# Kernel optimization log

Measured on AMD Instinct MI355X. Metric: run time of the kernel, lower is better.

Reference implementation:

```python
import jax, jax.numpy as jnp
import numpy as np

D = 1024
H = 16
DH = D // H
SCALE = 1.0 / float(np.sqrt(DH))
EPS = 1e-5


def layer_norm(x, g, b):
    mu = jnp.mean(x, axis=-1, keepdims=True)
    var = jnp.mean((x - mu) ** 2, axis=-1, keepdims=True)
    return (x - mu) * jax.lax.rsqrt(var + EPS) * g + b


def setup_inputs() -> dict:
    key = jax.random.key(0)
    ks = jax.random.split(key, 12)
    B, N = 2, 2048
    x = jax.random.normal(ks[0], (B, N, D), dtype=jnp.float32)
    # sparse 0/1 adjacency (tree-like density) plus self loops
    adj = (jax.random.uniform(ks[1], (B, N, N)) < 0.002).astype(jnp.float32)
    adj = jnp.maximum(adj, jnp.eye(N, dtype=jnp.float32)[None])
    attn_mask = jnp.zeros((B, N, N), dtype=jnp.float32)
    s = 0.02
    params = {
        "qkv_w": jax.random.normal(ks[2], (D, 3 * D)) * s,
        "qkv_b": jnp.zeros((3 * D,), jnp.float32),
        "out_w": jax.random.normal(ks[3], (D, D)) * s,
        "out_b": jnp.zeros((D,), jnp.float32),
        "ln1_g": jnp.ones((D,), jnp.float32),
        "ln1_b": jnp.zeros((D,), jnp.float32),
        "ln2_g": jnp.ones((D,), jnp.float32),
        "ln2_b": jnp.zeros((D,), jnp.float32),
        "ff1_w": jax.random.normal(ks[4], (D, 4 * D)) * s,
        "ff1_b": jnp.zeros((4 * D,), jnp.float32),
        "ff2_w": jax.random.normal(ks[5], (4 * D, D)) * s,
        "ff2_b": jnp.zeros((D,), jnp.float32),
        "struct_bias": jnp.zeros((1,), jnp.float32) + 0.1,
    }
    return {"x": x, "adjacency": adj, "attn_mask": attn_mask, **params}


def reference(x, adjacency, attn_mask, qkv_w, qkv_b, out_w, out_b,
              ln1_g, ln1_b, ln2_g, ln2_b, ff1_w, ff1_b, ff2_w, ff2_b,
              struct_bias):
    b, n, d = x.shape
    residual = x
    h = layer_norm(x, ln1_g, ln1_b)
    qkv = (h @ qkv_w + qkv_b).reshape(b, n, 3, H, DH)
    q = jnp.transpose(qkv[:, :, 0], (0, 2, 1, 3))  # [B,H,N,Dh]
    k = jnp.transpose(qkv[:, :, 1], (0, 2, 1, 3))
    v = jnp.transpose(qkv[:, :, 2], (0, 2, 1, 3))
    scores = jnp.einsum("bhqd,bhkd->bhqk", q, k) * SCALE
    scores = scores + struct_bias[0] * adjacency[:, None] + attn_mask[:, None]
    attn = jax.nn.softmax(scores, axis=-1)  # dropout is identity at eval
    out = jnp.einsum("bhqk,bhkd->bhqd", attn, v)
    out = jnp.transpose(out, (0, 2, 1, 3)).reshape(b, n, d)
    out = out @ out_w + out_b
    x1 = residual + out
    h2 = layer_norm(x1, ln2_g, ln2_b)
    ff = jax.nn.gelu(h2 @ ff1_w + ff1_b, approximate=False) @ ff2_w + ff2_b
    return x1 + ff
```

## Files before the change

### kernel.cpp

```cpp
#include <hip/hip_runtime.h>
#include <math.h>

#define Dm 1024
#define Hh 16
#define DHh 64
#define Bb 2
#define Nn 2048
#define Rr 4096
#define SCALE_ 0.125f
#define EPS_ 1e-5f
#define SMAX_ 4.0f
#define LOG2E_ 1.4426950408889634f

typedef unsigned short u16;
typedef __attribute__((ext_vector_type(8))) short short8;
typedef __attribute__((ext_vector_type(4))) float f32x4;

__device__ __forceinline__ u16 f2bf(float f) {
  union { float f; unsigned u; } v; v.f = f;
  unsigned r = v.u + 0x7fffu + ((v.u >> 16) & 1u);
  return (u16)(r >> 16);
}
__device__ __forceinline__ u16 f2bf_t(float f) {
  union { float f; unsigned u; } v; v.f = f;
  return (u16)(v.u >> 16);
}
__device__ __forceinline__ float bf2f(u16 h) {
  union { unsigned u; float f; } v; v.u = ((unsigned)h) << 16;
  return v.f;
}

__device__ __forceinline__ void g2l16(const u16* g, const u16* l) {
  __builtin_amdgcn_global_load_lds(
      (const __attribute__((address_space(1))) void*)g,
      (__attribute__((address_space(3))) void*)l, 16, 0, 0);
}

__global__ void transpose_all(const float* __restrict__ qkv_w, const float* __restrict__ out_w,
                              const float* __restrict__ ff1_w, const float* __restrict__ ff2_w,
                              u16* __restrict__ qkvT, u16* __restrict__ outT,
                              u16* __restrict__ ff1T, u16* __restrict__ ff2T) {
  __shared__ float tile[32][33];
  int flat = blockIdx.x;
  const float* W; u16* WT; int K, N, local;
  if (flat < 3072)        { W = qkv_w; WT = qkvT; K = 1024; N = 3072; local = flat; }
  else if (flat < 4096)   { W = out_w; WT = outT; K = 1024; N = 1024; local = flat - 3072; }
  else if (flat < 8192)   { W = ff1_w; WT = ff1T; K = 1024; N = 4096; local = flat - 4096; }
  else                    { W = ff2_w; WT = ff2T; K = 4096; N = 1024; local = flat - 8192; }
  int nx = N / 32;
  int n0 = (local % nx) * 32, k0 = (local / nx) * 32;
  int tx = threadIdx.x, ty = threadIdx.y;
#pragma unroll
  for (int i = 0; i < 4; i++)
    tile[ty + 8 * i][tx] = W[(size_t)(k0 + ty + 8 * i) * N + n0 + tx];
  __syncthreads();
#pragma unroll
  for (int i = 0; i < 4; i++)
    WT[(size_t)(n0 + ty + 8 * i) * K + k0 + tx] = f2bf(tile[tx][ty + 8 * i]);
}

__global__ void bias_precompute(const float* __restrict__ adj, const float* __restrict__ mask,
                                const float* __restrict__ sbp, u16* __restrict__ bias16) {
  const float sb = sbp[0];
  size_t i = ((size_t)blockIdx.x * 256 + threadIdx.x) * 8;
  float4 a0 = *(const float4*)(adj + i);
  float4 a1 = *(const float4*)(adj + i + 4);
  float4 m0 = *(const float4*)(mask + i);
  float4 m1 = *(const float4*)(mask + i + 4);
  ushort4 o0, o1;
  o0.x = f2bf(sb * a0.x + m0.x); o0.y = f2bf(sb * a0.y + m0.y);
  o0.z = f2bf(sb * a0.z + m0.z); o0.w = f2bf(sb * a0.w + m0.w);
  o1.x = f2bf(sb * a1.x + m1.x); o1.y = f2bf(sb * a1.y + m1.y);
  o1.z = f2bf(sb * a1.z + m1.z); o1.w = f2bf(sb * a1.w + m1.w);
  *(ushort4*)(bias16 + i) = o0;
  *(ushort4*)(bias16 + i + 4) = o1;
}

template <int BI>
__global__ void ln_kernel(const void* __restrict__ xin, const float* __restrict__ g,
                          const float* __restrict__ be, u16* __restrict__ out) {
  int row = blockIdx.x;
  int t = threadIdx.x;
  float4 v;
  if (BI) {
    ushort4 uv = ((const ushort4*)((const u16*)xin + (size_t)row * Dm))[t];
    v.x = bf2f(uv.x); v.y = bf2f(uv.y); v.z = bf2f(uv.z); v.w = bf2f(uv.w);
  } else {
    v = ((const float4*)((const float*)xin + (size_t)row * Dm))[t];
  }
  float s = v.x + v.y + v.z + v.w;
  float s2 = v.x * v.x + v.y * v.y + v.z * v.z + v.w * v.w;
#pragma unroll
  for (int o = 32; o > 0; o >>= 1) { s += __shfl_down(s, o); s2 += __shfl_down(s2, o); }
  __shared__ float sm[8];
  int w = t >> 6;
  if ((t & 63) == 0) { sm[w] = s; sm[4 + w] = s2; }
  __syncthreads();
  if (t == 0) {
    float a = sm[0] + sm[1] + sm[2] + sm[3];
    float a2 = sm[4] + sm[5] + sm[6] + sm[7];
    float mu = a * (1.f / Dm);
    sm[0] = mu;
    sm[1] = rsqrtf(a2 * (1.f / Dm) - mu * mu + EPS_);
  }
  __syncthreads();
  float mu = sm[0], rstd = sm[1];
  float4 gv = ((const float4*)g)[t];
  float4 bv = ((const float4*)be)[t];
  ushort4 o4;
  o4.x = f2bf((v.x - mu) * rstd * gv.x + bv.x);
  o4.y = f2bf((v.y - mu) * rstd * gv.y + bv.y);
  o4.z = f2bf((v.z - mu) * rstd * gv.z + bv.z);
  o4.w = f2bf((v.w - mu) * rstd * gv.w + bv.w);
  ((ushort4*)(out + (size_t)row * Dm))[t] = o4;
}

template <int MODE, int MI, int NI>
__global__ __launch_bounds__(256) void gemm_bt(
    const u16* __restrict__ A, const u16* __restrict__ BT,
    const float* __restrict__ bias, const void* __restrict__ res,
    void* __restrict__ Cout, u16* __restrict__ qb,
    u16* __restrict__ kb, u16* __restrict__ vb, int Ndim, int Kdim) {
  constexpr int TM = MI * 32, TN = NI * 32;
  constexpr int NS = (TM + TN) / 16;
  __shared__ u16 As[2][TM * 32];
  __shared__ u16 Bs[2][TN * 32];
  const int t = threadIdx.x;
  const int wave = t >> 6, lane = t & 63;
  const int wm = wave >> 1, wn = wave & 1;
  const int lr = lane & 15, lq = lane >> 4;
  const int flat = blockIdx.x + gridDim.x * blockIdx.y;
  constexpr int nMb = 4096 / TM;
  constexpr int mpx = nMb / 8;
  const int xcd = flat & 7;
  const int p = flat >> 3;
  const int m0 = (xcd * mpx + (p % mpx)) * TM;
  const int n0 = (p / mpx) * TN;

  auto stage = [&](int kt, int bsel) {
#pragma unroll
    for (int s = wave; s < NS; s += 4) {
      if (s < TM / 16)
        g2l16(A + (size_t)(m0 + s * 16 + (lane >> 2)) * Kdim + kt + (lane & 3) * 8,
              &As[bsel][(s * 16) * 32]);
      else
        g2l16(BT + (size_t)(n0 + (s - TM / 16) * 16 + (lane >> 2)) * Kdim + kt + (lane & 3) * 8,
              &Bs[bsel][((s - TM / 16) * 16) * 32]);
    }
  };

  f32x4 acc[MI][NI];
#pragma unroll
  for (int i = 0; i < MI; i++)
#pragma unroll
    for (int j = 0; j < NI; j++) acc[i][j] = (f32x4){0.f, 0.f, 0.f, 0.f};

  stage(0, 0);
  int cur = 0;
  for (int kt = 0; kt < Kdim; kt += 32) {
    __syncthreads();
    if (kt + 32 < Kdim) stage(kt + 32, cur ^ 1);
    short8 af[MI], bf[NI];
#pragma unroll
    for (int i = 0; i < MI; i++)
      af[i] = *(const short8*)&As[cur][(wm * (MI * 16) + i * 16 + lr) * 32 + lq * 8];
#pragma unroll
    for (int j = 0; j < NI; j++)
      bf[j] = *(const short8*)&Bs[cur][(wn * (NI * 16) + j * 16 + lr) * 32 + lq * 8];
#pragma unroll
    for (int i = 0; i < MI; i++)
#pragma unroll
      for (int j = 0; j < NI; j++)
        acc[i][j] = __builtin_amdgcn_mfma_f32_16x16x32_bf16(af[i], bf[j], acc[i][j], 0, 0, 0);
    cur ^= 1;
  }

#pragma unroll
  for (int i = 0; i < MI; i++) {
#pragma unroll
    for (int j = 0; j < NI; j++) {
#pragma unroll
      for (int r = 0; r < 4; r++) {
        int row = m0 + wm * (MI * 16) + i * 16 + lq * 4 + r;
        int col = n0 + wn * (NI * 16) + j * 16 + lr;
        float val = acc[i][j][r] + bias[col];
        if (MODE == 0) {
          int s = col >> 10, rem = col & 1023;
          int hh = rem >> 6, dh = rem & 63;
          int bi = row >> 11, ni = row & 2047;
          if (s == 2) {
            vb[(((size_t)bi * Hh + hh) * DHh + dh) * Nn + ni] = f2bf(val);
          } else {
            u16* dst = (s == 0) ? qb : kb;
            dst[(((size_t)bi * Hh + hh) * Nn + ni) * DHh + dh] = f2bf(val);
          }
        } else if (MODE == 1) {
          size_t o = (size_t)row * Ndim + col;
          ((u16*)Cout)[o] = f2bf(val + ((const float*)res)[o]);
        } else if (MODE == 3) {
          size_t o = (size_t)row * Ndim + col;
          ((float*)Cout)[o] = val + bf2f(((const u16*)res)[o]);
        } else {
          float u = val;
          float y2 = 1.5957691216f * fmaf(0.044715f * u, u * u, u);
          float gv = u / (1.f + __expf(-y2));
          size_t o = (size_t)row * Ndim + col;
          ((u16*)Cout)[o] = f2bf(gv);
        }
      }
    }
  }
}

__global__ __launch_bounds__(256) void attn_kernel(
    const u16* __restrict__ q, const u16* __restrict__ k, const u16* __restrict__ vT,
    const u16* __restrict__ bias16, u16* __restrict__ pO0, u16* __restrict__ pO1,
    float* __restrict__ pl) {
  const int qt = blockIdx.x, hb = blockIdx.y, kp = blockIdx.z;
  const int hh = hb & 15, b = hb >> 4;
  const int t = threadIdx.x, wave = t >> 6, lane = t & 63;
  const int lr = lane & 15, lq = lane >> 4;
  const size_t head_off = (((size_t)b * Hh + hh) * Nn) * DHh;
  const u16* Q = q + head_off;
  const u16* K = k + head_off;
  const u16* Vt = vT + head_off;
  const int q0 = qt * 128;
  const int kbase = kp * (Nn / 2);
  u16* pO = kp ? pO1 : pO0;

  __shared__ u16 Ks[64 * 72];
  __shared__ u16 VsT[64 * 72];
  __shared__ u16 Ps[4][32 * 72];

  short8 qf[2][2];
#pragma unroll
  for (int qs = 0; qs < 2; qs++) {
    const u16* Qr = Q + (size_t)(q0 + wave * 32 + qs * 16 + lr) * DHh;
    qf[qs][0] = *(const short8*)(Qr + lq * 8);
    qf[qs][1] = *(const short8*)(Qr + 32 + lq * 8);
  }
  f32x4 o_acc[2][4];
  float l_acc[2][4];
#pragma unroll
  for (int qs = 0; qs < 2; qs++) {
#pragma unroll
    for (int j = 0; j < 4; j++) o_acc[qs][j] = (f32x4){0.f, 0.f, 0.f, 0.f};
#pragma unroll
    for (int r = 0; r < 4; r++) l_acc[qs][r] = 0.f;
  }

  const int srow = t >> 2;
  const int sc0 = (t & 3) * 16;
  const int ssw = ((srow >> 2) & 3) << 4;
  const int wc0 = sc0 ^ ssw, wc1 = (sc0 + 8) ^ ssw;
  const u16* Kst = K + (size_t)srow * DHh + sc0;
  const u16* Vst = Vt + (size_t)srow * Nn + sc0;
  const int rsw = ((lr >> 2) & 3) << 4;

  const u16* bp = bias16 + ((size_t)b * Nn + q0 + wave * 32 + lq * 4) * Nn + lr;

  f32x4 kr0 = *(const f32x4*)(Kst + (size_t)kbase * DHh);
  f32x4 kr1 = *(const f32x4*)(Kst + (size_t)kbase * DHh + 8);
  f32x4 vr0 = *(const f32x4*)(Vst + kbase);
  f32x4 vr1 = *(const f32x4*)(Vst + kbase + 8);
  unsigned short bw[2][4][4];
#pragma unroll
  for (int qs = 0; qs < 2; qs++)
#pragma unroll
    for (int ns = 0; ns < 4; ns++)
#pragma unroll
      for (int r = 0; r < 4; r++)
        bw[qs][ns][r] = bp[(size_t)(qs * 16 + r) * Nn + kbase + ns * 16];

  const float C1 = SCALE_ * LOG2E_;
  const float C3 = -SMAX_ * LOG2E_;
  const int kend = kbase + Nn / 2;

  for (int kt = kbase; kt < kend; kt += 64) {
    __syncthreads();
    *(f32x4*)&Ks[srow * 72 + wc0] = kr0;
    *(f32x4*)&Ks[srow * 72 + wc1] = kr1;
    *(f32x4*)&VsT[srow * 72 + wc0] = vr0;
    *(f32x4*)&VsT[srow * 72 + wc1] = vr1;
    __syncthreads();
    if (kt + 64 < kend) {
      kr0 = *(const f32x4*)(Kst + (size_t)(kt + 64) * DHh);
      kr1 = *(const f32x4*)(Kst + (size_t)(kt + 64) * DHh + 8);
      vr0 = *(const f32x4*)(Vst + kt + 64);
      vr1 = *(const f32x4*)(Vst + kt + 64 + 8);
    }
    short8 kf[4][2];
#pragma unroll
    for (int ns = 0; ns < 4; ns++) {
      int row = ns * 16 + lr;
      kf[ns][0] = *(const short8*)&Ks[row * 72 + ((lq * 8) ^ rsw)];
      kf[ns][1] = *(const short8*)&Ks[row * 72 + ((32 + lq * 8) ^ rsw)];
    }
    f32x4 s0[4], s1[4];
#pragma unroll
    for (int ns = 0; ns < 4; ns++) {
      s0[ns] = (f32x4){0.f, 0.f, 0.f, 0.f};
      s1[ns] = (f32x4){0.f, 0.f, 0.f, 0.f};
      s0[ns] = __builtin_amdgcn_mfma_f32_16x16x32_bf16(qf[0][0], kf[ns][0], s0[ns], 0, 0, 0);
      s0[ns] = __builtin_amdgcn_mfma_f32_16x16x32_bf16(qf[0][1], kf[ns][1], s0[ns], 0, 0, 0);
      s1[ns] = __builtin_amdgcn_mfma_f32_16x16x32_bf16(qf[1][0], kf[ns][0], s1[ns], 0, 0, 0);
      s1[ns] = __builtin_amdgcn_mfma_f32_16x16x32_bf16(qf[1][1], kf[ns][1], s1[ns], 0, 0, 0);
    }
    float p0[4][4], p1[4][4];
#pragma unroll
    for (int ns = 0; ns < 4; ns++)
#pragma unroll
      for (int r = 0; r < 4; r++) {
        p0[ns][r] = exp2f(fmaf(s0[ns][r], C1, fmaf(bf2f(bw[0][ns][r]), LOG2E_, C3)));
        p1[ns][r] = exp2f(fmaf(s1[ns][r], C1, fmaf(bf2f(bw[1][ns][r]), LOG2E_, C3)));
        l_acc[0][r] += p0[ns][r];
        l_acc[1][r] += p1[ns][r];
      }
    if (kt + 64 < kend) {
#pragma unroll
      for (int qs = 0; qs < 2; qs++)
#pragma unroll
        for (int ns = 0; ns < 4; ns++)
#pragma unroll
          for (int r = 0; r < 4; r++)
            bw[qs][ns][r] = bp[(size_t)(qs * 16 + r) * Nn + kt + 64 + ns * 16];
    }
#pragma unroll
    for (int ns = 0; ns < 4; ns++) {
      int csw = ((ns ^ lq) << 4) + lr;
#pragma unroll
      for (int r = 0; r < 4; r++) {
        Ps[wave][(lq * 4 + r) * 72 + csw] = f2bf_t(p0[ns][r]);
        Ps[wave][(16 + lq * 4 + r) * 72 + csw] = f2bf_t(p1[ns][r]);
      }
    }
    short8 pf[2][2];
#pragma unroll
    for (int qs = 0; qs < 2; qs++) {
      pf[qs][0] = *(const short8*)&Ps[wave][(qs * 16 + lr) * 72 + ((lq * 8) ^ rsw)];
      pf[qs][1] = *(const short8*)&Ps[wave][(qs * 16 + lr) * 72 + ((32 + lq * 8) ^ rsw)];
    }
#pragma unroll
    for (int j = 0; j < 4; j++) {
      int row = j * 16 + lr;
      short8 vf0 = *(const short8*)&VsT[row * 72 + ((lq * 8) ^ rsw)];
      short8 vf1 = *(const short8*)&VsT[row * 72 + ((32 + lq * 8) ^ rsw)];
      o_acc[0][j] = __builtin_amdgcn_mfma_f32_16x16x32_bf16(pf[0][0], vf0, o_acc[0][j], 0, 0, 0);
      o_acc[0][j] = __builtin_amdgcn_mfma_f32_16x16x32_bf16(pf[0][1], vf1, o_acc[0][j], 0, 0, 0);
      o_acc[1][j] = __builtin_amdgcn_mfma_f32_16x16x32_bf16(pf[1][0], vf0, o_acc[1][j], 0, 0, 0);
      o_acc[1][j] = __builtin_amdgcn_mfma_f32_16x16x32_bf16(pf[1][1], vf1, o_acc[1][j], 0, 0, 0);
    }
  }
#pragma unroll
  for (int qs = 0; qs < 2; qs++)
#pragma unroll
    for (int r = 0; r < 4; r++) {
#pragma unroll
      for (int o = 1; o < 16; o <<= 1) l_acc[qs][r] += __shfl_xor(l_acc[qs][r], o);
      int qrow = q0 + wave * 32 + qs * 16 + lq * 4 + r;
      if (lr == 0)
        pl[((size_t)(kp * Bb + b) * Hh + hh) * Nn + qrow] = l_acc[qs][r];
#pragma unroll
      for (int j = 0; j < 4; j++) {
        pO[((size_t)(b * Nn + qrow)) * Dm + hh * DHh + j * 16 + lr] =
            f2bf(o_acc[qs][j][r]);
      }
    }
}

__global__ void attn_combine(const u16* __restrict__ pO0, const u16* __restrict__ pO1,
                             const float* __restrict__ pl, u16* __restrict__ ao) {
  int row = blockIdx.x;
  int t = threadIdx.x;
  int col = t * 4;
  int b = row >> 11, n = row & 2047, hh = col >> 6;
  size_t li = ((size_t)b * Hh + hh) * Nn + n;
  float inv = 1.f / (pl[li] + pl[(size_t)Bb * Hh * Nn + li]);
  ushort4 a0 = *(const ushort4*)(pO0 + (size_t)row * Dm + col);
  ushort4 a1 = *(const ushort4*)(pO1 + (size_t)row * Dm + col);
  ushort4 o;
  o.x = f2bf((bf2f(a0.x) + bf2f(a1.x)) * inv);
  o.y = f2bf((bf2f(a0.y) + bf2f(a1.y)) * inv);
  o.z = f2bf((bf2f(a0.z) + bf2f(a1.z)) * inv);
  o.w = f2bf((bf2f(a0.w) + bf2f(a1.w)) * inv);
  *(ushort4*)(ao + (size_t)row * Dm + col) = o;
}

extern "C" void kernel_launch(void* const* d_in, const int* in_sizes, int n_in,
                              void* d_out, int out_size, void* d_ws, size_t ws_size,
                              hipStream_t stream) {
  const float* x     = (const float*)d_in[0];
  const float* adj   = (const float*)d_in[1];
  const float* amask = (const float*)d_in[2];
  const float* qkv_w = (const float*)d_in[3];
  const float* qkv_b = (const float*)d_in[4];
  const float* out_w = (const float*)d_in[5];
  const float* out_b = (const float*)d_in[6];
  const float* ln1_g = (const float*)d_in[7];
  const float* ln1_b = (const float*)d_in[8];
  const float* ln2_g = (const float*)d_in[9];
  const float* ln2_b = (const float*)d_in[10];
  const float* ff1_w = (const float*)d_in[11];
  const float* ff1_b = (const float*)d_in[12];
  const float* ff2_w = (const float*)d_in[13];
  const float* ff2_b = (const float*)d_in[14];
  const float* sbias = (const float*)d_in[15];

  char* w = (char*)d_ws;
  const size_t MB = 1024 * 1024;
  u16* h      = (u16*)(w);
  u16* qb     = (u16*)(w + 8 * MB);
  u16* kb     = (u16*)(w + 16 * MB);
  u16* vb     = (u16*)(w + 24 * MB);
  u16* ao     = (u16*)(w + 32 * MB);
  float* pl   = (float*)(w + 40 * MB);
  u16* x1     = (u16*)(w + 40 * MB);
  u16* pO0    = (u16*)(w + 48 * MB);
  u16* pO1    = h;
  u16* qkvT   = (u16*)(w + 56 * MB);
  u16* outT   = (u16*)(w + 62 * MB);
  u16* ff1T   = (u16*)(w + 64 * MB);
  u16* ff2T   = (u16*)(w + 72 * MB);
  u16* bias16 = (u16*)(w + 80 * MB);
  u16* ffo    = qb;

  transpose_all<<<dim3(12288), dim3(32, 8), 0, stream>>>(
      qkv_w, out_w, ff1_w, ff2_w, qkvT, outT, ff1T, ff2T);

  bias_precompute<<<dim3((Bb * Nn * Nn) / (8 * 256)), dim3(256), 0, stream>>>(adj, amask, sbias, bias16);

  ln_kernel<0><<<dim3(Rr), dim3(256), 0, stream>>>(x, ln1_g, ln1_b, h);

  gemm_bt<0, 4, 4><<<dim3(3072 / 128, 4096 / 128), dim3(256), 0, stream>>>(
      h, qkvT, qkv_b, nullptr, nullptr, qb, kb, vb, 3072, 1024);

  attn_kernel<<<dim3(16, 32, 2), dim3(256), 0, stream>>>(qb, kb, vb, bias16, pO0, pO1, pl);

  attn_combine<<<dim3(Rr), dim3(256), 0, stream>>>(pO0, pO1, pl, ao);

  gemm_bt<1, 2, 2><<<dim3(1024 / 64, 4096 / 64), dim3(256), 0, stream>>>(
      ao, outT, out_b, x, (void*)x1, nullptr, nullptr, nullptr, 1024, 1024);

  ln_kernel<1><<<dim3(Rr), dim3(256), 0, stream>>>(x1, ln2_g, ln2_b, h);

  gemm_bt<2, 4, 4><<<dim3(4096 / 128, 4096 / 128), dim3(256), 0, stream>>>(
      h, ff1T, ff1_b, nullptr, (void*)ffo, nullptr, nullptr, nullptr, 4096, 1024);

  gemm_bt<3, 2, 2><<<dim3(1024 / 64, 4096 / 64), dim3(256), 0, stream>>>(
      ffo, ff2T, ff2_b, x1, d_out, nullptr, nullptr, nullptr, 1024, 4096);
}
```

Before: 464.0 us.

## Transpose QK^T MFMA operands, vectorize bias loads and P stores, retile output GEMMs

Swaps the operand order in the score MFMAs so each lane holds four consecutive key columns for a single query row. The bias can then be loaded as one ushort4 per fragment instead of scalar loads, and P written to LDS as packed uint2. The row-sum reduction shrinks from a 16-way shuffle per row to two shuffles. The log2e scaling and softmax offset are folded into the precomputed bias, which removes an FMA per element. The out-proj and FF2 GEMMs move to 128-row tiles with half as many blocks. The risks are bf16 rounding of the folded bias constant and lower occupancy for the larger GEMM tiles.

```diff
diff --git a/kernel.cpp b/kernel.cpp
--- a/kernel.cpp
+++ b/kernel.cpp
@@ -21,13 +21,13 @@
   unsigned r = v.u + 0x7fffu + ((v.u >> 16) & 1u);
   return (u16)(r >> 16);
 }
-__device__ __forceinline__ u16 f2bf_t(float f) {
-  union { float f; unsigned u; } v; v.f = f;
-  return (u16)(v.u >> 16);
-}
 __device__ __forceinline__ float bf2f(u16 h) {
   union { unsigned u; float f; } v; v.u = ((unsigned)h) << 16;
   return v.f;
+}
+__device__ __forceinline__ unsigned pk2(float a, float b) {
+  union { float f; unsigned u; } x, y; x.f = a; y.f = b;
+  return (x.u >> 16) | (y.u & 0xffff0000u);
 }
 
 __device__ __forceinline__ void g2l16(const u16* g, const u16* l) {
@@ -62,16 +62,21 @@
 __global__ void bias_precompute(const float* __restrict__ adj, const float* __restrict__ mask,
                                 const float* __restrict__ sbp, u16* __restrict__ bias16) {
   const float sb = sbp[0];
+  const float C3 = -SMAX_ * LOG2E_;
   size_t i = ((size_t)blockIdx.x * 256 + threadIdx.x) * 8;
   float4 a0 = *(const float4*)(adj + i);
   float4 a1 = *(const float4*)(adj + i + 4);
   float4 m0 = *(const float4*)(mask + i);
   float4 m1 = *(const float4*)(mask + i + 4);
   ushort4 o0, o1;
-  o0.x = f2bf(sb * a0.x + m0.x); o0.y = f2bf(sb * a0.y + m0.y);
-  o0.z = f2bf(sb * a0.z + m0.z); o0.w = f2bf(sb * a0.w + m0.w);
-  o1.x = f2bf(sb * a1.x + m1.x); o1.y = f2bf(sb * a1.y + m1.y);
-  o1.z = f2bf(sb * a1.z + m1.z); o1.w = f2bf(sb * a1.w + m1.w);
+  o0.x = f2bf(fmaf(fmaf(sb, a0.x, m0.x), LOG2E_, C3));
+  o0.y = f2bf(fmaf(fmaf(sb, a0.y, m0.y), LOG2E_, C3));
+  o0.z = f2bf(fmaf(fmaf(sb, a0.z, m0.z), LOG2E_, C3));
+  o0.w = f2bf(fmaf(fmaf(sb, a0.w, m0.w), LOG2E_, C3));
+  o1.x = f2bf(fmaf(fmaf(sb, a1.x, m1.x), LOG2E_, C3));
+  o1.y = f2bf(fmaf(fmaf(sb, a1.y, m1.y), LOG2E_, C3));
+  o1.z = f2bf(fmaf(fmaf(sb, a1.z, m1.z), LOG2E_, C3));
+  o1.w = f2bf(fmaf(fmaf(sb, a1.w, m1.w), LOG2E_, C3));
   *(ushort4*)(bias16 + i) = o0;
   *(ushort4*)(bias16 + i + 4) = o1;
 }
@@ -240,13 +245,12 @@
     qf[qs][1] = *(const short8*)(Qr + 32 + lq * 8);
   }
   f32x4 o_acc[2][4];
-  float l_acc[2][4];
+  float l_acc[2];
 #pragma unroll
   for (int qs = 0; qs < 2; qs++) {
 #pragma unroll
     for (int j = 0; j < 4; j++) o_acc[qs][j] = (f32x4){0.f, 0.f, 0.f, 0.f};
-#pragma unroll
-    for (int r = 0; r < 4; r++) l_acc[qs][r] = 0.f;
+    l_acc[qs] = 0.f;
   }
 
   const int srow = t >> 2;
@@ -257,23 +261,20 @@
   const u16* Vst = Vt + (size_t)srow * Nn + sc0;
   const int rsw = ((lr >> 2) & 3) << 4;
 
-  const u16* bp = bias16 + ((size_t)b * Nn + q0 + wave * 32 + lq * 4) * Nn + lr;
+  const u16* bp = bias16 + ((size_t)b * Nn + q0 + wave * 32 + lr) * Nn;
 
   f32x4 kr0 = *(const f32x4*)(Kst + (size_t)kbase * DHh);
   f32x4 kr1 = *(const f32x4*)(Kst + (size_t)kbase * DHh + 8);
   f32x4 vr0 = *(const f32x4*)(Vst + kbase);
   f32x4 vr1 = *(const f32x4*)(Vst + kbase + 8);
-  unsigned short bw[2][4][4];
+  ushort4 bw[2][4];
 #pragma unroll
   for (int qs = 0; qs < 2; qs++)
 #pragma unroll
     for (int ns = 0; ns < 4; ns++)
-#pragma unroll
-      for (int r = 0; r < 4; r++)
-        bw[qs][ns][r] = bp[(size_t)(qs * 16 + r) * Nn + kbase + ns * 16];
+      bw[qs][ns] = *(const ushort4*)(bp + (size_t)qs * 16 * Nn + kbase + ns * 16 + lq * 4);
 
   const float C1 = SCALE_ * LOG2E_;
-  const float C3 = -SMAX_ * LOG2E_;
   const int kend = kbase + Nn / 2;
 
   for (int kt = kbase; kt < kend; kt += 64) {
@@ -299,40 +300,41 @@
     f32x4 s0[4], s1[4];
 #pragma unroll
     for (int ns = 0; ns < 4; ns++) {
-      s0[ns] = (f32x4){0.f, 0.f, 0.f, 0.f};
-      s1[ns] = (f32x4){0.f, 0.f, 0.f, 0.f};
-      s0[ns] = __builtin_amdgcn_mfma_f32_16x16x32_bf16(qf[0][0], kf[ns][0], s0[ns], 0, 0, 0);
-      s0[ns] = __builtin_amdgcn_mfma_f32_16x16x32_bf16(qf[0][1], kf[ns][1], s0[ns], 0, 0, 0);
-      s1[ns] = __builtin_amdgcn_mfma_f32_16x16x32_bf16(qf[1][0], kf[ns][0], s1[ns], 0, 0, 0);
-      s1[ns] = __builtin_amdgcn_mfma_f32_16x16x32_bf16(qf[1][1], kf[ns][1], s1[ns], 0, 0, 0);
+      f32x4 z = (f32x4){0.f, 0.f, 0.f, 0.f};
+      s0[ns] = __builtin_amdgcn_mfma_f32_16x16x32_bf16(kf[ns][0], qf[0][0], z, 0, 0, 0);
+      s0[ns] = __builtin_amdgcn_mfma_f32_16x16x32_bf16(kf[ns][1], qf[0][1], s0[ns], 0, 0, 0);
+      s1[ns] = __builtin_amdgcn_mfma_f32_16x16x32_bf16(kf[ns][0], qf[1][0], z, 0, 0, 0);
+      s1[ns] = __builtin_amdgcn_mfma_f32_16x16x32_bf16(kf[ns][1], qf[1][1], s1[ns], 0, 0, 0);
     }
     float p0[4][4], p1[4][4];
 #pragma unroll
-    for (int ns = 0; ns < 4; ns++)
-#pragma unroll
-      for (int r = 0; r < 4; r++) {
-        p0[ns][r] = exp2f(fmaf(s0[ns][r], C1, fmaf(bf2f(bw[0][ns][r]), LOG2E_, C3)));
-        p1[ns][r] = exp2f(fmaf(s1[ns][r], C1, fmaf(bf2f(bw[1][ns][r]), LOG2E_, C3)));
-        l_acc[0][r] += p0[ns][r];
-        l_acc[1][r] += p1[ns][r];
-      }
+    for (int ns = 0; ns < 4; ns++) {
+      p0[ns][0] = exp2f(fmaf(s0[ns][0], C1, bf2f(bw[0][ns].x)));
+      p0[ns][1] = exp2f(fmaf(s0[ns][1], C1, bf2f(bw[0][ns].y)));
+      p0[ns][2] = exp2f(fmaf(s0[ns][2], C1, bf2f(bw[0][ns].z)));
+      p0[ns][3] = exp2f(fmaf(s0[ns][3], C1, bf2f(bw[0][ns].w)));
+      p1[ns][0] = exp2f(fmaf(s1[ns][0], C1, bf2f(bw[1][ns].x)));
+      p1[ns][1] = exp2f(fmaf(s1[ns][1], C1, bf2f(bw[1][ns].y)));
+      p1[ns][2] = exp2f(fmaf(s1[ns][2], C1, bf2f(bw[1][ns].z)));
+      p1[ns][3] = exp2f(fmaf(s1[ns][3], C1, bf2f(bw[1][ns].w)));
+      l_acc[0] += (p0[ns][0] + p0[ns][1]) + (p0[ns][2] + p0[ns][3]);
+      l_acc[1] += (p1[ns][0] + p1[ns][1]) + (p1[ns][2] + p1[ns][3]);
+    }
     if (kt + 64 < kend) {
 #pragma unroll
       for (int qs = 0; qs < 2; qs++)
 #pragma unroll
         for (int ns = 0; ns < 4; ns++)
-#pragma unroll
-          for (int r = 0; r < 4; r++)
-            bw[qs][ns][r] = bp[(size_t)(qs * 16 + r) * Nn + kt + 64 + ns * 16];
+          bw[qs][ns] = *(const ushort4*)(bp + (size_t)qs * 16 * Nn + kt + 64 + ns * 16 + lq * 4);
     }
 #pragma unroll
     for (int ns = 0; ns < 4; ns++) {
-      int csw = ((ns ^ lq) << 4) + lr;
-#pragma unroll
-      for (int r = 0; r < 4; r++) {
-        Ps[wave][(lq * 4 + r) * 72 + csw] = f2bf_t(p0[ns][r]);
-        Ps[wave][(16 + lq * 4 + r) * 72 + csw] = f2bf_t(p1[ns][r]);
-      }
+      int sc = ((ns ^ ((lr >> 2) & 3)) << 4) + lq * 4;
+      uint2 w0, w1;
+      w0.x = pk2(p0[ns][0], p0[ns][1]); w0.y = pk2(p0[ns][2], p0[ns][3]);
+      w1.x = pk2(p1[ns][0], p1[ns][1]); w1.y = pk2(p1[ns][2], p1[ns][3]);
+      *(uint2*)&Ps[wave][lr * 72 + sc] = w0;
+      *(uint2*)&Ps[wave][(16 + lr) * 72 + sc] = w1;
     }
     short8 pf[2][2];
 #pragma unroll
@@ -352,20 +354,22 @@
     }
   }
 #pragma unroll
-  for (int qs = 0; qs < 2; qs++)
+  for (int qs = 0; qs < 2; qs++) {
+    float l = l_acc[qs];
+    l += __shfl_xor(l, 16);
+    l += __shfl_xor(l, 32);
+    if (lane < 16)
+      pl[((size_t)(kp * Bb + b) * Hh + hh) * Nn + q0 + wave * 32 + qs * 16 + lr] = l;
 #pragma unroll
     for (int r = 0; r < 4; r++) {
-#pragma unroll
-      for (int o = 1; o < 16; o <<= 1) l_acc[qs][r] += __shfl_xor(l_acc[qs][r], o);
       int qrow = q0 + wave * 32 + qs * 16 + lq * 4 + r;
-      if (lr == 0)
-        pl[((size_t)(kp * Bb + b) * Hh + hh) * Nn + qrow] = l_acc[qs][r];
 #pragma unroll
       for (int j = 0; j < 4; j++) {
         pO[((size_t)(b * Nn + qrow)) * Dm + hh * DHh + j * 16 + lr] =
             f2bf(o_acc[qs][j][r]);
       }
     }
+  }
 }
 
 __global__ void attn_combine(const u16* __restrict__ pO0, const u16* __restrict__ pO1,
@@ -438,7 +442,7 @@
 
   attn_combine<<<dim3(Rr), dim3(256), 0, stream>>>(pO0, pO1, pl, ao);
 
-  gemm_bt<1, 2, 2><<<dim3(1024 / 64, 4096 / 64), dim3(256), 0, stream>>>(
+  gemm_bt<1, 4, 2><<<dim3(1024 / 64, 4096 / 128), dim3(256), 0, stream>>>(
       ao, outT, out_b, x, (void*)x1, nullptr, nullptr, nullptr, 1024, 1024);
 
   ln_kernel<1><<<dim3(Rr), dim3(256), 0, stream>>>(x1, ln2_g, ln2_b, h);
@@ -446,6 +450,6 @@
   gemm_bt<2, 4, 4><<<dim3(4096 / 128, 4096 / 128), dim3(256), 0, stream>>>(
       h, ff1T, ff1_b, nullptr, (void*)ffo, nullptr, nullptr, nullptr, 4096, 1024);
 
-  gemm_bt<3, 2, 2><<<dim3(1024 / 64, 4096 / 64), dim3(256), 0, stream>>>(
+  gemm_bt<3, 4, 2><<<dim3(1024 / 64, 4096 / 128), dim3(256), 0, stream>>>(
       ffo, ff2T, ff2_b, x1, d_out, nullptr, nullptr, nullptr, 1024, 4096);
 }
```

Result: no change. 464.6 us (+0.1%).
